# Kernel optimization log

Hardware: AMD Instinct MI355X
Metric: run time of the kernel (lower is better)

Reference implementation:

```python
import jax, jax.numpy as jnp
import numpy as np

N = 20000      # number of boxes / graph nodes
E = 160000     # random edges (before self-loops)
DIM = 1024     # feature dim (SIA default)


def setup_inputs() -> dict:
    key = jax.random.key(0)
    ks = jax.random.split(key, 12)
    feats = jax.random.normal(ks[0], (N, DIM), dtype=jnp.float32)
    boxes = jax.random.uniform(ks[1], (N, 4), dtype=jnp.float32)
    src = jax.random.randint(ks[2], (E,), 0, N, dtype=jnp.int32)
    dst = jax.random.randint(ks[3], (E,), 0, N, dtype=jnp.int32)
    loop = jnp.arange(N, dtype=jnp.int32)
    # dgl.add_self_loop: every node gets a self edge
    edges_src = jnp.concatenate([src, loop])
    edges_dst = jnp.concatenate([dst, loop])
    s = 0.02
    return {
        'feats': feats, 'boxes': boxes,
        'edges_src': edges_src, 'edges_dst': edges_dst,
        'w_pos1': jax.random.normal(ks[4], (4, DIM), jnp.float32) * s,
        'b_pos1': jnp.zeros((DIM,), jnp.float32),
        'w_pos2': jax.random.normal(ks[5], (DIM, DIM), jnp.float32) * s,
        'b_pos2': jnp.zeros((DIM,), jnp.float32),
        'w_g1': jax.random.normal(ks[6], (DIM, DIM), jnp.float32) * s,
        'b_g1': jnp.zeros((DIM,), jnp.float32),
        'w_g2': jax.random.normal(ks[7], (DIM, DIM), jnp.float32) * s,
        'b_g2': jnp.zeros((DIM,), jnp.float32),
    }


def _graph_conv(h, src, dst, w, b, n):
    # DGL GraphConv, norm='both', in_feats == out_feats => aggregate then matmul.
    ones = jnp.ones(src.shape, dtype=h.dtype)
    out_deg = jax.ops.segment_sum(ones, src, num_segments=n)
    in_deg = jax.ops.segment_sum(ones, dst, num_segments=n)
    norm_src = jnp.where(out_deg > 0, jax.lax.rsqrt(jnp.maximum(out_deg, 1.0)), 0.0)
    norm_dst = jnp.where(in_deg > 0, jax.lax.rsqrt(jnp.maximum(in_deg, 1.0)), 0.0)
    h = h * norm_src[:, None]
    agg = jax.ops.segment_sum(h[src], dst, num_segments=n)  # irregular gather/scatter
    agg = agg * norm_dst[:, None]
    return agg @ w + b


def reference(feats, boxes, edges_src, edges_dst,
              w_pos1, b_pos1, w_pos2, b_pos2,
              w_g1, b_g1, w_g2, b_g2):
    n = feats.shape[0]
    boxes = jnp.clip(boxes, -10.0, 10.0)
    pos = jax.nn.relu(boxes @ w_pos1 + b_pos1) @ w_pos2 + b_pos2
    h = feats + pos
    h = _graph_conv(h, edges_src, edges_dst, w_g1, b_g1, n)
    h = jax.nn.relu(h)  # dropout is identity in eval
    h = _graph_conv(h, edges_src, edges_dst, w_g2, b_g2, n)
    return h.mean(0)  # frame token [DIM]
```

## Files before the change

### kernel.cpp

```cpp
#include <hip/hip_runtime.h>
#include <hip/hip_bf16.h>
#include <stdint.h>

#define DIM 1024

typedef __attribute__((ext_vector_type(4))) float f32x4;
typedef __attribute__((ext_vector_type(8))) short short8;
typedef __attribute__((ext_vector_type(4))) short short4v;

__device__ __forceinline__ float bf2f(ushort u) {
    union { uint32_t u; float f; } c; c.u = ((uint32_t)u) << 16; return c.f;
}
__device__ __forceinline__ ushort f2bf(float f) {
    union { float f; uint32_t u; } c; c.f = f;
    uint32_t r = (c.u + 0x7fffu + ((c.u >> 16) & 1u)) >> 16;
    return (ushort)r;
}

__device__ __forceinline__ void async_copy16(void* lds, const void* g) {
    __builtin_amdgcn_global_load_lds((const __attribute__((address_space(1))) void*)g,
                                     (__attribute__((address_space(3))) void*)lds, 16, 0, 0);
}


__global__ void deg_kernel(const int* __restrict__ src, const int* __restrict__ dst,
                           int* out_deg, int* in_deg, int ee) {
    int e = blockIdx.x * 256 + threadIdx.x;
    if (e < ee) {
        atomicAdd(&out_deg[src[e]], 1);
        atomicAdd(&in_deg[dst[e]], 1);
    }
}

__global__ void norm_kernel(const int* __restrict__ out_deg, const int* __restrict__ in_deg,
                            float* ns, float* nd, int n) {
    int i = blockIdx.x * 256 + threadIdx.x;
    if (i < n) {
        int od = out_deg[i], id = in_deg[i];
        ns[i] = od > 0 ? rsqrtf((float)od) : 0.f;
        nd[i] = id > 0 ? rsqrtf((float)id) : 0.f;
    }
}

__global__ void csum_kernel(const int* __restrict__ src, const int* __restrict__ dst,
                            const float* __restrict__ nd, float* cw, int ee) {
    int e = blockIdx.x * 256 + threadIdx.x;
    if (e < ee) atomicAdd(&cw[src[e]], nd[dst[e]]);
}

__global__ void scan_kernel(const int* __restrict__ deg, int* row_ptr, int n) {
    __shared__ int buf[1024];
    __shared__ int carry;
    int tid = threadIdx.x;
    if (tid == 0) carry = 0;
    __syncthreads();
    for (int base = 0; base < n; base += 1024) {
        int x = (base + tid < n) ? deg[base + tid] : 0;
        buf[tid] = x;
        __syncthreads();
        for (int off = 1; off < 1024; off <<= 1) {
            int v = (tid >= off) ? buf[tid - off] : 0;
            __syncthreads();
            buf[tid] += v;
            __syncthreads();
        }
        if (base + tid < n) row_ptr[base + tid] = carry + buf[tid] - x;
        __syncthreads();
        if (tid == 0) carry += buf[1023];
        __syncthreads();
    }
}

__global__ void wnode_cursor_kernel(float* cw, const float* __restrict__ ns,
                                    const int* __restrict__ row_ptr, int* cursor, int n) {
    int i = blockIdx.x * 256 + threadIdx.x;
    if (i < n) {
        cw[i] *= ns[i];
        cursor[i] = row_ptr[i];
    }
}

__global__ void scatter_kernel(const int* __restrict__ src, const int* __restrict__ dst,
                               int* cursor, int* csr_src, int ee) {
    int e = blockIdx.x * 256 + threadIdx.x;
    if (e < ee) {
        int p = atomicAdd(&cursor[dst[e]], 1);
        csr_src[p] = src[e];
    }
}


__global__ __launch_bounds__(256) void posA_kernel(const float* __restrict__ boxes,
                                                   const float* __restrict__ w1,
                                                   const float* __restrict__ b1,
                                                   ushort* __restrict__ t, int n) {
    int row = blockIdx.x;
    if (row >= n) return;
    float b[4];
#pragma unroll
    for (int j = 0; j < 4; j++) {
        float v = boxes[row * 4 + j];
        b[j] = fminf(fmaxf(v, -10.f), 10.f);
    }
    int c0 = threadIdx.x * 4;
    short4v o;
#pragma unroll
    for (int q = 0; q < 4; q++) {
        int col = c0 + q;
        float v = b1[col];
#pragma unroll
        for (int j = 0; j < 4; j++) v = fmaf(b[j], w1[j * DIM + col], v);
        v = fmaxf(v, 0.f);
        o[q] = (short)f2bf(v);
    }
    *(short4v*)(t + (size_t)row * DIM + c0) = o;
}


__global__ __launch_bounds__(256) void transpose_bf16_kernel(const float* __restrict__ w,
                                                             ushort* __restrict__ wt) {
    __shared__ float tile[32][33];
    int bx = blockIdx.x, by = blockIdx.y;
    int tx = threadIdx.x & 31, ty = threadIdx.x >> 5;
#pragma unroll
    for (int r = 0; r < 32; r += 8)
        tile[ty + r][tx] = w[(size_t)(by * 32 + ty + r) * DIM + bx * 32 + tx];
    __syncthreads();
#pragma unroll
    for (int r = 0; r < 32; r += 8)
        wt[(size_t)(bx * 32 + ty + r) * DIM + by * 32 + tx] = f2bf(tile[tx][ty + r]);
}


template <int EPI>
__global__ __launch_bounds__(256) void gemm_kernel(
    const ushort* __restrict__ A, const ushort* __restrict__ Bt,
    const float* __restrict__ bias,
    const float* __restrict__ feats, const float* __restrict__ nsrc, ushort* __restrict__ hs,
    const float* __restrict__ wnode, float* __restrict__ vec,
    int mreal) {
    __shared__ __align__(128) ushort ldsA[128 * 64];
    __shared__ __align__(128) ushort ldsB[128 * 64];
    int tid = threadIdx.x, lane = tid & 63, wid = tid >> 6;
    int bm = blockIdx.x, bn = blockIdx.y;
    int wm = wid >> 1, wn = wid & 1;

    f32x4 acc[4][4];
#pragma unroll
    for (int m = 0; m < 4; m++)
#pragma unroll
        for (int n = 0; n < 4; n++) acc[m][n] = (f32x4){0.f, 0.f, 0.f, 0.f};

    int srow = wid * 8 + (lane >> 3);
    int sseg = (lane & 7) ^ (lane >> 3);
    const ushort* gA = A + (size_t)(bm * 128 + srow) * DIM + sseg * 8;
    const ushort* gB = Bt + (size_t)(bn * 128 + srow) * DIM + sseg * 8;
    ushort* lA = &ldsA[(wid * 8) * 64];
    ushort* lB = &ldsB[(wid * 8) * 64];

    int r16 = lane & 15, khi = lane >> 4, rx = lane & 7;

    for (int kt = 0; kt < DIM / 64; ++kt) {
        __syncthreads();
#pragma unroll
        for (int c = 0; c < 4; c++) {
            async_copy16(lA + c * 2048, gA + (size_t)c * 32 * DIM + kt * 64);
            async_copy16(lB + c * 2048, gB + (size_t)c * 32 * DIM + kt * 64);
        }
        asm volatile("s_waitcnt vmcnt(0)" ::: "memory");
        __syncthreads();
#pragma unroll
        for (int kk = 0; kk < 2; kk++) {
            short8 af[4], bfv[4];
#pragma unroll
            for (int m = 0; m < 4; m++) {
                int row = wm * 64 + m * 16 + r16;
                int seg = (kk * 4 + khi) ^ rx;
                af[m] = *(const short8*)&ldsA[row * 64 + seg * 8];
            }
#pragma unroll
            for (int n = 0; n < 4; n++) {
                int row = wn * 64 + n * 16 + r16;
                int seg = (kk * 4 + khi) ^ rx;
                bfv[n] = *(const short8*)&ldsB[row * 64 + seg * 8];
            }
#pragma unroll
            for (int m = 0; m < 4; m++)
#pragma unroll
                for (int n = 0; n < 4; n++)
                    acc[m][n] = __builtin_amdgcn_mfma_f32_16x16x32_bf16(af[m], bfv[n], acc[m][n], 0, 0, 0);
        }
    }

    int colbase = bn * 128 + wn * 64;
    int rowbase = bm * 128 + wm * 64 + khi * 4;
    if (EPI == 1) {
#pragma unroll
        for (int m = 0; m < 4; m++) {
#pragma unroll
            for (int j = 0; j < 4; j++) {
                int r = rowbase + m * 16 + j;
                if (r < mreal) {
                    float ns = nsrc[r];
#pragma unroll
                    for (int n = 0; n < 4; n++) {
                        int col = colbase + n * 16 + r16;
                        float v = acc[m][n][j] + bias[col] + feats[(size_t)r * DIM + col];
                        hs[(size_t)r * DIM + col] = f2bf(v * ns);
                    }
                }
            }
        }
    } else {
        float cs[4] = {0.f, 0.f, 0.f, 0.f};
#pragma unroll
        for (int m = 0; m < 4; m++) {
#pragma unroll
            for (int j = 0; j < 4; j++) {
                int r = rowbase + m * 16 + j;
                if (r < mreal) {
                    float w = wnode[r];
#pragma unroll
                    for (int n = 0; n < 4; n++) {
                        int col = colbase + n * 16 + r16;
                        float v = acc[m][n][j] + bias[col];
                        cs[n] += fmaxf(v, 0.f) * w;
                    }
                }
            }
        }
#pragma unroll
        for (int n = 0; n < 4; n++) {
            float s = cs[n];
            s += __shfl_xor(s, 16);
            s += __shfl_xor(s, 32);
            if (khi == 0) atomicAdd(&vec[colbase + n * 16 + r16], s);
        }
    }
}


__global__ __launch_bounds__(256) void agg_kernel(const ushort* __restrict__ hs,
                                                  const int* __restrict__ row_ptr,
                                                  const int* __restrict__ in_deg,
                                                  const int* __restrict__ csr_src,
                                                  const float* __restrict__ ndst,
                                                  ushort* __restrict__ aggn, int n) {
    int node = blockIdx.x * 4 + (threadIdx.x >> 6);
    if (node >= n) return;
    int lane = threadIdx.x & 63;
    int start = row_ptr[node], cnt = in_deg[node];
    float a0[8] = {0, 0, 0, 0, 0, 0, 0, 0};
    float a1[8] = {0, 0, 0, 0, 0, 0, 0, 0};
    for (int e = 0; e < cnt; e++) {
        const ushort* rp = hs + (size_t)csr_src[start + e] * DIM;
        short8 v0 = *(const short8*)(rp + lane * 8);
        short8 v1 = *(const short8*)(rp + 512 + lane * 8);
#pragma unroll
        for (int t = 0; t < 8; t++) {
            a0[t] += bf2f((ushort)v0[t]);
            a1[t] += bf2f((ushort)v1[t]);
        }
    }
    float nd = ndst[node];
    short8 o0, o1;
#pragma unroll
    for (int t = 0; t < 8; t++) {
        o0[t] = (short)f2bf(a0[t] * nd);
        o1[t] = (short)f2bf(a1[t] * nd);
    }
    *(short8*)(aggn + (size_t)node * DIM + lane * 8) = o0;
    *(short8*)(aggn + (size_t)node * DIM + 512 + lane * 8) = o1;
}


__global__ __launch_bounds__(256) void final_kernel(const float* __restrict__ vec,
                                                    const float* __restrict__ w2,
                                                    const float* __restrict__ b2,
                                                    float* out, float invn) {
    int d = blockIdx.x * 256 + threadIdx.x;
    int kb = blockIdx.y * 128;
    float acc = 0.f;
#pragma unroll 4
    for (int k = 0; k < 128; k++) acc = fmaf(vec[kb + k], w2[(size_t)(kb + k) * DIM + d], acc);
    float add = acc * invn + (blockIdx.y == 0 ? b2[d] : 0.f);
    atomicAdd(&out[d], add);
}


extern "C" void kernel_launch(void* const* d_in, const int* in_sizes, int n_in,
                              void* d_out, int out_size, void* d_ws, size_t ws_size,
                              hipStream_t stream) {
    const float* feats  = (const float*)d_in[0];
    const float* boxes  = (const float*)d_in[1];
    const int*   esrc   = (const int*)d_in[2];
    const int*   edst   = (const int*)d_in[3];
    const float* w_pos1 = (const float*)d_in[4];
    const float* b_pos1 = (const float*)d_in[5];
    const float* w_pos2 = (const float*)d_in[6];
    const float* b_pos2 = (const float*)d_in[7];
    const float* w_g1   = (const float*)d_in[8];
    const float* b_g1   = (const float*)d_in[9];
    const float* w_g2   = (const float*)d_in[10];
    const float* b_g2   = (const float*)d_in[11];

    int n = in_sizes[0] / DIM;
    int ee = in_sizes[2];
    int mtiles = (n + 127) / 128;
    char* p = (char*)d_ws;
    auto alloc = [&](size_t bytes) -> char* {
        char* r = p;
        p += (bytes + 255) & ~((size_t)255);
        return r;
    };
    size_t mp = (size_t)mtiles * 128;
    ushort* t_aggn = (ushort*)alloc(mp * DIM * 2);
    ushort* hs     = (ushort*)alloc(mp * DIM * 2);
    ushort* wt1    = (ushort*)alloc((size_t)DIM * DIM * 2);
    ushort* wt2    = (ushort*)alloc((size_t)DIM * DIM * 2);
    char* zero_base = p;
    int*   out_deg = (int*)alloc((size_t)n * 4);
    int*   in_deg  = (int*)alloc((size_t)n * 4);
    float* cw      = (float*)alloc((size_t)n * 4);
    float* vec     = (float*)alloc((size_t)DIM * 4);
    size_t zero_bytes = (size_t)(p - zero_base);
    float* nsrc    = (float*)alloc((size_t)n * 4);
    float* ndst    = (float*)alloc((size_t)n * 4);
    int*   row_ptr = (int*)alloc((size_t)(n + 1) * 4);
    int*   cursor  = (int*)alloc((size_t)n * 4);
    int*   csr_src = (int*)alloc((size_t)ee * 4);

    hipMemsetAsync(zero_base, 0, zero_bytes, stream);
    hipMemsetAsync(d_out, 0, (size_t)out_size * 4, stream);

    int eb = (ee + 255) / 256;
    int nb = (n + 255) / 256;

    deg_kernel<<<eb, 256, 0, stream>>>(esrc, edst, out_deg, in_deg, ee);
    posA_kernel<<<n, 256, 0, stream>>>(boxes, w_pos1, b_pos1, t_aggn, n);
    transpose_bf16_kernel<<<dim3(32, 32), 256, 0, stream>>>(w_pos2, wt1);
    transpose_bf16_kernel<<<dim3(32, 32), 256, 0, stream>>>(w_g1, wt2);
    norm_kernel<<<nb, 256, 0, stream>>>(out_deg, in_deg, nsrc, ndst, n);
    csum_kernel<<<eb, 256, 0, stream>>>(esrc, edst, ndst, cw, ee);
    scan_kernel<<<1, 1024, 0, stream>>>(in_deg, row_ptr, n);
    wnode_cursor_kernel<<<nb, 256, 0, stream>>>(cw, nsrc, row_ptr, cursor, n);
    scatter_kernel<<<eb, 256, 0, stream>>>(esrc, edst, cursor, csr_src, ee);

    gemm_kernel<1><<<dim3(mtiles, 8), 256, 0, stream>>>(t_aggn, wt1, b_pos2, feats, nsrc, hs,
                                                        nullptr, nullptr, n);
    agg_kernel<<<(n + 3) / 4, 256, 0, stream>>>(hs, row_ptr, in_deg, csr_src, ndst, t_aggn, n);
    gemm_kernel<2><<<dim3(mtiles, 8), 256, 0, stream>>>(t_aggn, wt2, b_g1, nullptr, nullptr,
                                                        nullptr, cw, vec, n);
    final_kernel<<<dim3(4, 8), 256, 0, stream>>>(vec, w_g2, b_g2, (float*)d_out,
                                                 1.0f / (float)n);
}
```

Baseline: 450.6 us.

## Reorder graph conv to matmul-then-aggregate, double-buffer GEMM, XCD-aware tiling, shuffle scan

Layer 1 is reordered so the GEMM with w_g1 runs on the normalized features first, and the gather-aggregate then runs on the GEMM output. The aggregate kernel is fused with bias, ReLU, the per-node weight and the column reduction into vec, using a persistent grid of 1024 blocks, two-edge unrolling and an LDS reduction. The GEMM gains LDS double buffering to overlap global-to-LDS loads with MFMA work, plus a 1D grid remapped so that consecutive blocks on the same XCD share A rows. The scan switches from LDS Hillis-Steele to wave shuffles. Aggregating after the matmul rounds the GEMM output to bf16 before summation, which changes numerics slightly, and doubling the LDS buffers may reduce occupancy.

```diff
diff --git a/kernel.cpp b/kernel.cpp
--- a/kernel.cpp
+++ b/kernel.cpp
@@ -49,24 +49,35 @@
 }
 
 __global__ void scan_kernel(const int* __restrict__ deg, int* row_ptr, int n) {
-    __shared__ int buf[1024];
-    __shared__ int carry;
-    int tid = threadIdx.x;
-    if (tid == 0) carry = 0;
+    __shared__ int wsum[16];
+    __shared__ int carry_s;
+    int tid = threadIdx.x, lane = tid & 63, wid = tid >> 6;
+    if (tid == 0) carry_s = 0;
     __syncthreads();
     for (int base = 0; base < n; base += 1024) {
         int x = (base + tid < n) ? deg[base + tid] : 0;
-        buf[tid] = x;
+        int v = x;
+#pragma unroll
+        for (int off = 1; off < 64; off <<= 1) {
+            int u = __shfl_up(v, off);
+            if (lane >= off) v += u;
+        }
+        if (lane == 63) wsum[wid] = v;
         __syncthreads();
-        for (int off = 1; off < 1024; off <<= 1) {
-            int v = (tid >= off) ? buf[tid - off] : 0;
-            __syncthreads();
-            buf[tid] += v;
-            __syncthreads();
-        }
-        if (base + tid < n) row_ptr[base + tid] = carry + buf[tid] - x;
+        if (wid == 0 && lane < 16) {
+            int wv = wsum[lane];
+#pragma unroll
+            for (int off = 1; off < 16; off <<= 1) {
+                int wu = __shfl_up(wv, off);
+                if (lane >= off) wv += wu;
+            }
+            wsum[lane] = wv;
+        }
         __syncthreads();
-        if (tid == 0) carry += buf[1023];
+        int waveoff = (wid > 0) ? wsum[wid - 1] : 0;
+        if (base + tid < n) row_ptr[base + tid] = carry_s + waveoff + v - x;
+        __syncthreads();
+        if (tid == 0) carry_s += wsum[15];
         __syncthreads();
     }
 }
@@ -135,14 +146,18 @@
 template <int EPI>
 __global__ __launch_bounds__(256) void gemm_kernel(
     const ushort* __restrict__ A, const ushort* __restrict__ Bt,
-    const float* __restrict__ bias,
-    const float* __restrict__ feats, const float* __restrict__ nsrc, ushort* __restrict__ hs,
-    const float* __restrict__ wnode, float* __restrict__ vec,
-    int mreal) {
-    __shared__ __align__(128) ushort ldsA[128 * 64];
-    __shared__ __align__(128) ushort ldsB[128 * 64];
+    const float* __restrict__ bias, const float* __restrict__ feats,
+    const float* __restrict__ nsrc, ushort* __restrict__ outp,
+    int mtiles, int mreal) {
+    __shared__ __align__(128) ushort ldsA[2][128 * 64];
+    __shared__ __align__(128) ushort ldsB[2][128 * 64];
+    int j = blockIdx.x;
+    int xcd = j & 7, k = j >> 3;
+    int bm = xcd + 8 * (k >> 3);
+    int bn = k & 7;
+    if (bm >= mtiles) return;
+
     int tid = threadIdx.x, lane = tid & 63, wid = tid >> 6;
-    int bm = blockIdx.x, bn = blockIdx.y;
     int wm = wid >> 1, wn = wid & 1;
 
     f32x4 acc[4][4];
@@ -155,20 +170,25 @@
     int sseg = (lane & 7) ^ (lane >> 3);
     const ushort* gA = A + (size_t)(bm * 128 + srow) * DIM + sseg * 8;
     const ushort* gB = Bt + (size_t)(bn * 128 + srow) * DIM + sseg * 8;
-    ushort* lA = &ldsA[(wid * 8) * 64];
-    ushort* lB = &ldsB[(wid * 8) * 64];
 
     int r16 = lane & 15, khi = lane >> 4, rx = lane & 7;
 
-    for (int kt = 0; kt < DIM / 64; ++kt) {
-        __syncthreads();
+    auto stage = [&](int buf, int kt) {
+        ushort* lA = &ldsA[buf][(wid * 8) * 64];
+        ushort* lB = &ldsB[buf][(wid * 8) * 64];
 #pragma unroll
         for (int c = 0; c < 4; c++) {
             async_copy16(lA + c * 2048, gA + (size_t)c * 32 * DIM + kt * 64);
             async_copy16(lB + c * 2048, gB + (size_t)c * 32 * DIM + kt * 64);
         }
-        asm volatile("s_waitcnt vmcnt(0)" ::: "memory");
-        __syncthreads();
+    };
+
+    stage(0, 0);
+    asm volatile("s_waitcnt vmcnt(0)" ::: "memory");
+    __syncthreads();
+    int cur = 0;
+    for (int kt = 0; kt < DIM / 64; ++kt) {
+        if (kt < DIM / 64 - 1) stage(cur ^ 1, kt + 1);
 #pragma unroll
         for (int kk = 0; kk < 2; kk++) {
             short8 af[4], bfv[4];
@@ -176,19 +196,24 @@
             for (int m = 0; m < 4; m++) {
                 int row = wm * 64 + m * 16 + r16;
                 int seg = (kk * 4 + khi) ^ rx;
-                af[m] = *(const short8*)&ldsA[row * 64 + seg * 8];
+                af[m] = *(const short8*)&ldsA[cur][row * 64 + seg * 8];
             }
 #pragma unroll
             for (int n = 0; n < 4; n++) {
                 int row = wn * 64 + n * 16 + r16;
                 int seg = (kk * 4 + khi) ^ rx;
-                bfv[n] = *(const short8*)&ldsB[row * 64 + seg * 8];
+                bfv[n] = *(const short8*)&ldsB[cur][row * 64 + seg * 8];
             }
 #pragma unroll
             for (int m = 0; m < 4; m++)
 #pragma unroll
                 for (int n = 0; n < 4; n++)
                     acc[m][n] = __builtin_amdgcn_mfma_f32_16x16x32_bf16(af[m], bfv[n], acc[m][n], 0, 0, 0);
+        }
+        if (kt < DIM / 64 - 1) {
+            asm volatile("s_waitcnt vmcnt(0)" ::: "memory");
+            __syncthreads();
+            cur ^= 1;
         }
     }
 
@@ -198,79 +223,104 @@
 #pragma unroll
         for (int m = 0; m < 4; m++) {
 #pragma unroll
-            for (int j = 0; j < 4; j++) {
-                int r = rowbase + m * 16 + j;
+            for (int jj = 0; jj < 4; jj++) {
+                int r = rowbase + m * 16 + jj;
                 if (r < mreal) {
                     float ns = nsrc[r];
 #pragma unroll
                     for (int n = 0; n < 4; n++) {
                         int col = colbase + n * 16 + r16;
-                        float v = acc[m][n][j] + bias[col] + feats[(size_t)r * DIM + col];
-                        hs[(size_t)r * DIM + col] = f2bf(v * ns);
+                        float v = acc[m][n][jj] + bias[col] + feats[(size_t)r * DIM + col];
+                        outp[(size_t)r * DIM + col] = f2bf(v * ns);
                     }
                 }
             }
         }
     } else {
-        float cs[4] = {0.f, 0.f, 0.f, 0.f};
 #pragma unroll
         for (int m = 0; m < 4; m++) {
 #pragma unroll
-            for (int j = 0; j < 4; j++) {
-                int r = rowbase + m * 16 + j;
+            for (int jj = 0; jj < 4; jj++) {
+                int r = rowbase + m * 16 + jj;
                 if (r < mreal) {
-                    float w = wnode[r];
 #pragma unroll
                     for (int n = 0; n < 4; n++) {
                         int col = colbase + n * 16 + r16;
-                        float v = acc[m][n][j] + bias[col];
-                        cs[n] += fmaxf(v, 0.f) * w;
+                        outp[(size_t)r * DIM + col] = f2bf(acc[m][n][jj]);
                     }
                 }
             }
         }
-#pragma unroll
-        for (int n = 0; n < 4; n++) {
-            float s = cs[n];
-            s += __shfl_xor(s, 16);
-            s += __shfl_xor(s, 32);
-            if (khi == 0) atomicAdd(&vec[colbase + n * 16 + r16], s);
-        }
-    }
-}
-
-
-__global__ __launch_bounds__(256) void agg_kernel(const ushort* __restrict__ hs,
-                                                  const int* __restrict__ row_ptr,
-                                                  const int* __restrict__ in_deg,
-                                                  const int* __restrict__ csr_src,
-                                                  const float* __restrict__ ndst,
-                                                  ushort* __restrict__ aggn, int n) {
-    int node = blockIdx.x * 4 + (threadIdx.x >> 6);
-    if (node >= n) return;
-    int lane = threadIdx.x & 63;
-    int start = row_ptr[node], cnt = in_deg[node];
-    float a0[8] = {0, 0, 0, 0, 0, 0, 0, 0};
-    float a1[8] = {0, 0, 0, 0, 0, 0, 0, 0};
-    for (int e = 0; e < cnt; e++) {
-        const ushort* rp = hs + (size_t)csr_src[start + e] * DIM;
-        short8 v0 = *(const short8*)(rp + lane * 8);
-        short8 v1 = *(const short8*)(rp + 512 + lane * 8);
-#pragma unroll
-        for (int t = 0; t < 8; t++) {
-            a0[t] += bf2f((ushort)v0[t]);
-            a1[t] += bf2f((ushort)v1[t]);
-        }
-    }
-    float nd = ndst[node];
-    short8 o0, o1;
-#pragma unroll
-    for (int t = 0; t < 8; t++) {
-        o0[t] = (short)f2bf(a0[t] * nd);
-        o1[t] = (short)f2bf(a1[t] * nd);
-    }
-    *(short8*)(aggn + (size_t)node * DIM + lane * 8) = o0;
-    *(short8*)(aggn + (size_t)node * DIM + 512 + lane * 8) = o1;
+    }
+}
+
+
+__global__ __launch_bounds__(256) void agg2_kernel(
+    const ushort* __restrict__ z, const int* __restrict__ row_ptr,
+    const int* __restrict__ in_deg, const int* __restrict__ csr_src,
+    const float* __restrict__ ndst, const float* __restrict__ wnode,
+    const float* __restrict__ bg1, float* __restrict__ vec, int n) {
+    __shared__ float red[DIM];
+    int lane = threadIdx.x & 63, wid = threadIdx.x >> 6;
+    int wave = blockIdx.x * 4 + wid;
+    int nwaves = gridDim.x * 4;
+    int c0 = lane * 8;
+
+    float bv[16];
+#pragma unroll
+    for (int t = 0; t < 8; t++) { bv[t] = bg1[c0 + t]; bv[8 + t] = bg1[512 + c0 + t]; }
+    float part[16];
+#pragma unroll
+    for (int t = 0; t < 16; t++) part[t] = 0.f;
+
+    for (int node = wave; node < n; node += nwaves) {
+        int start = row_ptr[node], cnt = in_deg[node];
+        float a[16];
+#pragma unroll
+        for (int t = 0; t < 16; t++) a[t] = 0.f;
+        int e = 0;
+        for (; e + 2 <= cnt; e += 2) {
+            const ushort* r0 = z + (size_t)csr_src[start + e] * DIM;
+            const ushort* r1 = z + (size_t)csr_src[start + e + 1] * DIM;
+            short8 v00 = *(const short8*)(r0 + c0);
+            short8 v01 = *(const short8*)(r0 + 512 + c0);
+            short8 v10 = *(const short8*)(r1 + c0);
+            short8 v11 = *(const short8*)(r1 + 512 + c0);
+#pragma unroll
+            for (int t = 0; t < 8; t++) {
+                a[t]     += bf2f((ushort)v00[t]) + bf2f((ushort)v10[t]);
+                a[8 + t] += bf2f((ushort)v01[t]) + bf2f((ushort)v11[t]);
+            }
+        }
+        if (e < cnt) {
+            const ushort* r0 = z + (size_t)csr_src[start + e] * DIM;
+            short8 v00 = *(const short8*)(r0 + c0);
+            short8 v01 = *(const short8*)(r0 + 512 + c0);
+#pragma unroll
+            for (int t = 0; t < 8; t++) {
+                a[t]     += bf2f((ushort)v00[t]);
+                a[8 + t] += bf2f((ushort)v01[t]);
+            }
+        }
+        float nd = ndst[node], w = wnode[node];
+#pragma unroll
+        for (int t = 0; t < 16; t++)
+            part[t] = fmaf(w, fmaxf(fmaf(nd, a[t], bv[t]), 0.f), part[t]);
+    }
+
+    if (wid == 0) {
+#pragma unroll
+        for (int t = 0; t < 8; t++) { red[c0 + t] = part[t]; red[512 + c0 + t] = part[8 + t]; }
+    }
+    __syncthreads();
+    for (int w = 1; w < 4; ++w) {
+        if (wid == w) {
+#pragma unroll
+            for (int t = 0; t < 8; t++) { red[c0 + t] += part[t]; red[512 + c0 + t] += part[8 + t]; }
+        }
+        __syncthreads();
+    }
+    for (int c = threadIdx.x; c < DIM; c += 256) atomicAdd(&vec[c], red[c]);
 }
 
 
@@ -307,6 +357,9 @@
     int n = in_sizes[0] / DIM;
     int ee = in_sizes[2];
     int mtiles = (n + 127) / 128;
+    int groups = (mtiles + 7) / 8;
+    int gemm_grid = groups * 64;
+
     char* p = (char*)d_ws;
     auto alloc = [&](size_t bytes) -> char* {
         char* r = p;
@@ -314,7 +367,7 @@
         return r;
     };
     size_t mp = (size_t)mtiles * 128;
-    ushort* t_aggn = (ushort*)alloc(mp * DIM * 2);
+    ushort* t_z    = (ushort*)alloc(mp * DIM * 2);
     ushort* hs     = (ushort*)alloc(mp * DIM * 2);
     ushort* wt1    = (ushort*)alloc((size_t)DIM * DIM * 2);
     ushort* wt2    = (ushort*)alloc((size_t)DIM * DIM * 2);
@@ -337,7 +390,7 @@
     int nb = (n + 255) / 256;
 
     deg_kernel<<<eb, 256, 0, stream>>>(esrc, edst, out_deg, in_deg, ee);
-    posA_kernel<<<n, 256, 0, stream>>>(boxes, w_pos1, b_pos1, t_aggn, n);
+    posA_kernel<<<n, 256, 0, stream>>>(boxes, w_pos1, b_pos1, t_z, n);
     transpose_bf16_kernel<<<dim3(32, 32), 256, 0, stream>>>(w_pos2, wt1);
     transpose_bf16_kernel<<<dim3(32, 32), 256, 0, stream>>>(w_g1, wt2);
     norm_kernel<<<nb, 256, 0, stream>>>(out_deg, in_deg, nsrc, ndst, n);
@@ -346,11 +399,8 @@
     wnode_cursor_kernel<<<nb, 256, 0, stream>>>(cw, nsrc, row_ptr, cursor, n);
     scatter_kernel<<<eb, 256, 0, stream>>>(esrc, edst, cursor, csr_src, ee);
 
-    gemm_kernel<1><<<dim3(mtiles, 8), 256, 0, stream>>>(t_aggn, wt1, b_pos2, feats, nsrc, hs,
-                                                        nullptr, nullptr, n);
-    agg_kernel<<<(n + 3) / 4, 256, 0, stream>>>(hs, row_ptr, in_deg, csr_src, ndst, t_aggn, n);
-    gemm_kernel<2><<<dim3(mtiles, 8), 256, 0, stream>>>(t_aggn, wt2, b_g1, nullptr, nullptr,
-                                                        nullptr, cw, vec, n);
-    final_kernel<<<dim3(4, 8), 256, 0, stream>>>(vec, w_g2, b_g2, (float*)d_out,
-                                                 1.0f / (float)n);
-}
+    gemm_kernel<1><<<gemm_grid, 256, 0, stream>>>(t_z, wt1, b_pos2, feats, nsrc, hs, mtiles, n);
+    gemm_kernel<0><<<gemm_grid, 256, 0, stream>>>(hs, wt2, nullptr, nullptr, nullptr, t_z, mtiles, n);
+    agg2_kernel<<<1024, 256, 0, stream>>>(t_z, row_ptr, in_deg, csr_src, ndst, cw, b_g1, vec, n);
+    final_kernel<<<dim3(4, 8), 256, 0, stream>>>(vec, w_g2, b_g2, (float*)d_out, 1.0f / (float)n);
+}
```

Result: no change. 449.2 us (-0.3%).
